# Optimization experiments

Hardware: AMD Instinct MI355X
Metric: run time of the kernel (lower is better)

The kernel has to match this reference:

```python
import jax, jax.numpy as jnp
import numpy as np

T, HID, H, HKV, D = 4096, 2048, 16, 2, 128
EPS = 1e-6


def setup_inputs() -> dict:
    key = jax.random.key(0)
    ks = jax.random.split(key, 5)
    hidden_states = jax.random.normal(ks[0], (T, HID), dtype=jnp.float32)
    # rope angles: build realistic cos/sin from positions and inv-freqs
    inv_freq = 1.0 / (10000.0 ** (jnp.arange(0, D, 2, dtype=jnp.float32) / D))
    ang = jnp.arange(T, dtype=jnp.float32)[:, None] * inv_freq[None, :]  # [T, D/2]
    ang = jnp.concatenate([ang, ang], axis=-1)  # [T, D]
    cos, sin = jnp.cos(ang), jnp.sin(ang)
    w_qkv = jax.random.normal(ks[1], (HID, (2 * H + 2 * HKV) * D), dtype=jnp.float32) * (HID ** -0.5)
    w_o = jax.random.normal(ks[2], (H * D, HID), dtype=jnp.float32) * ((H * D) ** -0.5)
    q_norm_w = jnp.ones((D,), dtype=jnp.float32)
    k_norm_w = jnp.ones((D,), dtype=jnp.float32)
    return {"hidden_states": hidden_states, "cos": cos, "sin": sin,
            "w_qkv": w_qkv, "w_o": w_o, "q_norm_w": q_norm_w, "k_norm_w": k_norm_w}


def _rms_norm(x, w):
    var = jnp.mean(x * x, axis=-1, keepdims=True)
    return x * jax.lax.rsqrt(var + EPS) * w


def _rotate_half(x):
    x1, x2 = x[..., : D // 2], x[..., D // 2:]
    return jnp.concatenate([-x2, x1], axis=-1)


def _rope(x, cos, sin):
    # x: [T, h, D]; cos/sin: [T, D]
    return x * cos[:, None, :] + _rotate_half(x) * sin[:, None, :]


def reference(hidden_states, cos, sin, w_qkv, w_o, q_norm_w, k_norm_w):
    qkv = hidden_states @ w_qkv  # [T, (2H+2HKV)*D]
    q_sz, kv_sz = 2 * H * D, HKV * D
    # packed query+gate: view as [T, H, 2D], first half query, second half gate
    qg = qkv[:, :q_sz].reshape(T, H, 2 * D)
    q, gate = qg[..., :D], qg[..., D:]
    k = qkv[:, q_sz:q_sz + kv_sz].reshape(T, HKV, D)
    v = qkv[:, q_sz + kv_sz:].reshape(T, HKV, D)
    q = _rms_norm(q, q_norm_w)
    k = _rms_norm(k, k_norm_w)
    q = _rope(q, cos, sin)
    k = _rope(k, cos, sin)
    # GQA: expand kv heads to H
    rep = H // HKV
    k = jnp.repeat(k, rep, axis=1)  # [T, H, D]
    v = jnp.repeat(v, rep, axis=1)
    scale = D ** -0.5
    scores = jnp.einsum('thd,shd->hts', q, k) * scale  # [H, T, T]
    causal = jnp.tril(jnp.ones((T, T), dtype=bool))
    scores = jnp.where(causal[None], scores, jnp.finfo(scores.dtype).min)
    probs = jax.nn.softmax(scores, axis=-1)
    attn = jnp.einsum('hts,shd->thd', probs, v)  # [T, H, D]
    out = attn.reshape(T, H * D) * jax.nn.sigmoid(gate.reshape(T, H * D))
    return out @ w_o
```

## Files before the change

kernel.cpp:

```cpp
#include <hip/hip_runtime.h>
#include <hip/hip_bf16.h>
#include <math.h>


namespace {
constexpr int kT   = 4096;
constexpr int kHid = 2048;
constexpr int kH   = 16;
constexpr int kHkv = 2;
constexpr int kD   = 128;
constexpr int kNqkv = (2 * kH + 2 * kHkv) * kD;
constexpr int kQsz  = 2 * kH * kD;
constexpr int kRowU = kNqkv * 2;
constexpr float kEps = 1e-6f;
constexpr float kScale = 0.08838834764831845f;
}

typedef __attribute__((ext_vector_type(8))) short short8;
typedef __attribute__((ext_vector_type(4))) float floatx4;

__device__ inline unsigned short f2bf(float x) {
  unsigned u = __float_as_uint(x);
  u = (u + 0x7fffu + ((u >> 16) & 1u)) >> 16;
  return (unsigned short)u;
}

__device__ inline void gload_lds16(const void* g, void* l) {
  typedef const __attribute__((address_space(1))) unsigned GQ;
  typedef __attribute__((address_space(3))) unsigned LQ;
  __builtin_amdgcn_global_load_lds((GQ*)g, (LQ*)l, 16, 0, 0);
}

__global__ __launch_bounds__(256)
void cvt_bf16(const float* __restrict__ in, unsigned short* __restrict__ out,
              long nelem) {
  long i = ((long)blockIdx.x * 256 + threadIdx.x) * 4;
  if (i >= nelem) return;
  float4 v = *(const float4*)(in + i);
  unsigned long long p = (unsigned long long)f2bf(v.x) |
                         ((unsigned long long)f2bf(v.y) << 16) |
                         ((unsigned long long)f2bf(v.z) << 32) |
                         ((unsigned long long)f2bf(v.w) << 48);
  *(unsigned long long*)(out + i) = p;
}

__global__ __launch_bounds__(256)
void transpose_cvt(const float* __restrict__ in, unsigned short* __restrict__ out,
                   int R, int C) {
  __shared__ float t[32][33];
  const int bx = blockIdx.x * 32;
  const int by = blockIdx.y * 32;
  const int x = threadIdx.x & 31, y = threadIdx.x >> 5;
#pragma unroll
  for (int j = 0; j < 4; ++j)
    t[y * 4 + j][x] = in[(long)(by + y * 4 + j) * C + bx + x];
  __syncthreads();
#pragma unroll
  for (int j = 0; j < 4; ++j)
    out[(long)(bx + y * 4 + j) * R + by + x] = f2bf(t[x][y * 4 + j]);
}

__global__ __launch_bounds__(256)
void vt_transpose(const float* __restrict__ qkv, unsigned short* __restrict__ VtG) {
  __shared__ float t[32][33];
  const int t0 = blockIdx.x * 32;
  const int c0 = blockIdx.y * 32;
  const int x = threadIdx.x & 31, y = threadIdx.x >> 5;
#pragma unroll
  for (int j = 0; j < 4; ++j)
    t[y * 4 + j][x] = qkv[(long)(t0 + y * 4 + j) * kNqkv + 4352 + c0 + x];
  __syncthreads();
#pragma unroll
  for (int j = 0; j < 4; ++j)
    VtG[(long)(c0 + y * 4 + j) * kT + t0 + x] = f2bf(t[x][y * 4 + j]);
}

__global__ __launch_bounds__(256)
void gemm_bf16(const unsigned short* __restrict__ A,
               const unsigned short* __restrict__ Bt, float* __restrict__ C,
               int M, int N, int K) {
  __shared__ __align__(16) unsigned short As[128 * 32];
  __shared__ __align__(16) unsigned short Bs[128 * 32];
  const int tid = threadIdx.x;
  const int lane = tid & 63;
  const int w = tid >> 6;
  const int wr = w >> 1, wc = w & 1;
  const int n = lane & 15;
  const int quad = lane >> 4;
  const long bm = (long)blockIdx.x * 128, bn = (long)blockIdx.y * 128;

  floatx4 acc[4][4];
  floatx4 zero = {0.f, 0.f, 0.f, 0.f};
#pragma unroll
  for (int a = 0; a < 4; ++a)
#pragma unroll
    for (int b = 0; b < 4; ++b) acc[a][b] = zero;

  for (int k0 = 0; k0 < K; k0 += 32) {
    __syncthreads();
#pragma unroll
    for (int it = 0; it < 2; ++it) {
      int ci = (w * 2 + it) * 64 + lane;
      int r = ci >> 2, c = ci & 3;
      int cg = c ^ ((r >> 1) & 3);
      gload_lds16(A + (bm + r) * (long)K + k0 + cg * 8, As + (w * 2 + it) * 512);
      gload_lds16(Bt + (bn + r) * (long)K + k0 + cg * 8, Bs + (w * 2 + it) * 512);
    }
    __syncthreads();

    short8 af[4], bf[4];
#pragma unroll
    for (int a = 0; a < 4; ++a) {
      int m = wr * 64 + a * 16 + n;
      af[a] = *(const short8*)(As + m * 32 + (quad ^ ((m >> 1) & 3)) * 8);
    }
#pragma unroll
    for (int b = 0; b < 4; ++b) {
      int nn = wc * 64 + b * 16 + n;
      bf[b] = *(const short8*)(Bs + nn * 32 + (quad ^ ((nn >> 1) & 3)) * 8);
    }
#pragma unroll
    for (int a = 0; a < 4; ++a)
#pragma unroll
      for (int b = 0; b < 4; ++b)
        acc[a][b] = __builtin_amdgcn_mfma_f32_16x16x32_bf16(af[a], bf[b], acc[a][b], 0, 0, 0);
  }
#pragma unroll
  for (int a = 0; a < 4; ++a)
#pragma unroll
    for (int b = 0; b < 4; ++b)
#pragma unroll
      for (int r = 0; r < 4; ++r)
        C[(bm + wr * 64 + a * 16 + quad * 4 + r) * (long)N + bn + wc * 64 + b * 16 + n] =
            acc[a][b][r];
}

__global__ __launch_bounds__(128)
void norm_rope_cvt(float* qkv, const float* __restrict__ cosb,
                   const float* __restrict__ sinb, const float* __restrict__ qw,
                   const float* __restrict__ kw) {
  unsigned short* qkvu = (unsigned short*)qkv;
  const int blk = blockIdx.x;
  const int t = blk / 18;
  const int h = blk % 18;
  const int i = threadIdx.x;

  const bool isq = (h < kH);
  const long base = (long)t * kNqkv + (isq ? h * 2 * kD : kQsz + (h - kH) * kD);
  float x = qkv[base + i];
  float v = x * x;
#pragma unroll
  for (int off = 1; off < 64; off <<= 1) v += __shfl_xor(v, off, 64);
  __shared__ float wsum[2];
  if ((i & 63) == 0) wsum[i >> 6] = v;
  __syncthreads();
  float rms = rsqrtf((wsum[0] + wsum[1]) * (1.0f / kD) + kEps);
  float nv = x * rms * (isq ? qw[i] : kw[i]);
  __shared__ float nb[128];
  nb[i] = nv;
  __syncthreads();
  float rot = (i < 64) ? -nb[i + 64] : nb[i - 64];
  float ro = nv * cosb[t * kD + i] + rot * sinb[t * kD + i];
  if (isq) {
    float g = qkv[base + kD + i];
    qkv[base + kD + i] = 1.0f / (1.0f + __expf(-g));
    qkvu[(long)t * kRowU + 512 * h + i] = f2bf(ro);
  } else {
    qkvu[(long)t * kRowU + 8192 + 256 * (h - kH) + i] = f2bf(ro);
  }
}

__global__ __launch_bounds__(256, 4)
void flash_attn_mfma(const unsigned short* qkvu, const float* qkvf,
                     const unsigned short* VtG, unsigned short* __restrict__ og) {
  __shared__ __align__(16) unsigned short Ks[64 * 128];
  __shared__ __align__(16) unsigned short Vt[128 * 64];

  const int tid = threadIdx.x;
  const int lane = tid & 63;
  const int w = tid >> 6;
  const int n = lane & 15;
  const int quad = lane >> 4;
  const int g = blockIdx.x;
  const int m = g & 63;
  const int bm = (m & 1) ? 63 - (m >> 1) : (m >> 1);
  const int h = g >> 6;
  const int hk = h >> 3;
  const int q0 = bm * 64;

  short8 qf[4];
  {
    const unsigned short* qrow = qkvu + (long)(q0 + 16 * w + n) * kRowU + 512 * h;
#pragma unroll
    for (int ks = 0; ks < 4; ++ks)
      qf[ks] = *(const short8*)(qrow + 32 * ks + 8 * quad);
  }
  short8 lfrag;
  {
    short o = (n == 0) ? (short)0x3F80 : (short)0;
    lfrag = (short8){o, o, o, o, o, o, o, o};
  }

  floatx4 O[8];
  floatx4 zero = {0.f, 0.f, 0.f, 0.f};
#pragma unroll
  for (int dt = 0; dt < 8; ++dt) O[dt] = zero;
  floatx4 Ol = zero;

  for (int kn = 0; kn <= bm; ++kn) {
    __syncthreads();
#pragma unroll
    for (int it = 0; it < 4; ++it) {
      int pc = (w * 4 + it) * 64 + lane;
      int r = pc >> 4, c = pc & 15;
      int lc = c ^ (r & 15);
      gload_lds16(qkvu + (long)(kn * 64 + r) * kRowU + 8192 + 256 * hk + 8 * lc,
                  Ks + (w * 4 + it) * 512);
    }
#pragma unroll
    for (int it = 0; it < 4; ++it) {
      int pc = (w * 4 + it) * 64 + lane;
      int d = pc >> 3, c = pc & 7;
      int lc = c ^ (d & 7);
      gload_lds16(VtG + (long)hk * (128 * kT) + (long)d * kT + kn * 64 + 8 * lc,
                  Vt + (w * 4 + it) * 512);
    }
    __syncthreads();

    floatx4 S[4];
#pragma unroll
    for (int ct = 0; ct < 4; ++ct) S[ct] = zero;
#pragma unroll
    for (int ks = 0; ks < 4; ++ks) {
#pragma unroll
      for (int ct = 0; ct < 4; ++ct) {
        int row = 16 * ct + n;
        short8 kf = *(const short8*)(Ks + row * 128 + ((4 * ks + quad) ^ n) * 8);
        S[ct] = __builtin_amdgcn_mfma_f32_16x16x32_bf16(qf[ks], kf, S[ct], 0, 0, 0);
      }
    }
    __syncthreads();

    unsigned short* Ps = Ks;
    const bool diag = (kn == bm);
    const int hi = n >> 3, lo = n & 7;
#pragma unroll
    for (int r = 0; r < 4; ++r) {
      int iloc = 16 * w + quad * 4 + r;
      float p0 = __expf(S[0][r] * kScale);
      float p1 = __expf(S[1][r] * kScale);
      float p2 = __expf(S[2][r] * kScale);
      float p3 = __expf(S[3][r] * kScale);
      if (diag) {
        if (n > iloc) p0 = 0.f;
        if (16 + n > iloc) p1 = 0.f;
        if (32 + n > iloc) p2 = 0.f;
        if (48 + n > iloc) p3 = 0.f;
      }
      int prow = 16 * w + quad * 4 + r;
      int sw = prow & 7;
      Ps[prow * 128 + (((0 + hi) ^ sw) << 3) + lo] = f2bf(p0);
      Ps[prow * 128 + (((2 + hi) ^ sw) << 3) + lo] = f2bf(p1);
      Ps[prow * 128 + (((4 + hi) ^ sw) << 3) + lo] = f2bf(p2);
      Ps[prow * 128 + (((6 + hi) ^ sw) << 3) + lo] = f2bf(p3);
    }
    __asm__ volatile("s_waitcnt lgkmcnt(0)" ::: "memory");

#pragma unroll
    for (int ks = 0; ks < 2; ++ks) {
      int rr = 16 * w + n;
      short8 pf = *(const short8*)(Ps + rr * 128 + (((4 * ks + quad) ^ (rr & 7)) << 3));
      Ol = __builtin_amdgcn_mfma_f32_16x16x32_bf16(pf, lfrag, Ol, 0, 0, 0);
#pragma unroll
      for (int dt = 0; dt < 8; ++dt) {
        int d = 16 * dt + n;
        short8 vf = *(const short8*)(Vt + d * 64 + (((4 * ks + quad) ^ (d & 7)) << 3));
        O[dt] = __builtin_amdgcn_mfma_f32_16x16x32_bf16(pf, vf, O[dt], 0, 0, 0);
      }
    }
  }

#pragma unroll
  for (int r = 0; r < 4; ++r) {
    float l = __shfl(Ol[r], quad << 4, 64);
    float inv = 1.0f / l;
    int row = q0 + 16 * w + quad * 4 + r;
#pragma unroll
    for (int dt = 0; dt < 8; ++dt) {
      int col = 16 * dt + n;
      float gte = qkvf[(long)row * kNqkv + 256 * h + 128 + col];
      og[(long)row * kHid + 128 * h + col] = f2bf(O[dt][r] * inv * gte);
    }
  }
}

extern "C" void kernel_launch(void* const* d_in, const int* in_sizes, int n_in,
                              void* d_out, int out_size, void* d_ws, size_t ws_size,
                              hipStream_t stream) {
  (void)in_sizes; (void)n_in; (void)out_size; (void)ws_size;
  const float* hs   = (const float*)d_in[0];
  const float* cosb = (const float*)d_in[1];
  const float* sinb = (const float*)d_in[2];
  const float* wqkv = (const float*)d_in[3];
  const float* wo   = (const float*)d_in[4];
  const float* qw   = (const float*)d_in[5];
  const float* kw   = (const float*)d_in[6];
  float* out = (float*)d_out;

  char* ws = (char*)d_ws;
  float* qkv = (float*)ws;
  unsigned short* hsb = (unsigned short*)(ws + 75497472);
  unsigned short* og  = hsb;
  unsigned short* wt  = (unsigned short*)(ws + 92274688);
  unsigned short* VtG = wt;

  cvt_bf16<<<dim3(8192), 256, 0, stream>>>(hs, hsb, (long)kT * kHid);
  transpose_cvt<<<dim3(kNqkv / 32, kHid / 32), 256, 0, stream>>>(wqkv, wt, kHid, kNqkv);
  gemm_bf16<<<dim3(kT / 128, kNqkv / 128), 256, 0, stream>>>(hsb, wt, qkv, kT, kNqkv, kHid);
  vt_transpose<<<dim3(kT / 32, 8), 256, 0, stream>>>(qkv, VtG);
  norm_rope_cvt<<<dim3(kT * 18), 128, 0, stream>>>(qkv, cosb, sinb, qw, kw);
  flash_attn_mfma<<<dim3(kT / 64 * kH), 256, 0, stream>>>((const unsigned short*)qkv, qkv, VtG, og);
  transpose_cvt<<<dim3(kHid / 32, kHid / 32), 256, 0, stream>>>(wo, wt, kHid, kHid);
  gemm_bf16<<<dim3(kT / 128, kHid / 128), 256, 0, stream>>>(og, wt, out, kT, kHid, kHid);
}
```

Baseline: 551.7 us.

## Double GEMM K-tile and widen attention query tile to 128 rows

The GEMM now stages 64-wide K slices per iteration with an 8-way XOR swizzle, which halves the number of barrier pairs per output tile. The attention kernel handles 128 query rows per block, two 16-row MFMA tiles per wave, so each K/V tile loaded into LDS feeds twice as many queries. Block order is changed to head-fastest with the longest causal rows scheduled first. The cost is more registers per thread (the occupancy hint of 4 is removed) and half as many attention blocks, which can hurt load balance and latency hiding.

```diff
diff --git a/kernel.cpp b/kernel.cpp
--- a/kernel.cpp
+++ b/kernel.cpp
@@ -79,8 +79,8 @@
 void gemm_bf16(const unsigned short* __restrict__ A,
                const unsigned short* __restrict__ Bt, float* __restrict__ C,
                int M, int N, int K) {
-  __shared__ __align__(16) unsigned short As[128 * 32];
-  __shared__ __align__(16) unsigned short Bs[128 * 32];
+  __shared__ __align__(16) unsigned short As[128 * 64];
+  __shared__ __align__(16) unsigned short Bs[128 * 64];
   const int tid = threadIdx.x;
   const int lane = tid & 63;
   const int w = tid >> 6;
@@ -96,34 +96,37 @@
 #pragma unroll
     for (int b = 0; b < 4; ++b) acc[a][b] = zero;
 
-  for (int k0 = 0; k0 < K; k0 += 32) {
-    __syncthreads();
-#pragma unroll
-    for (int it = 0; it < 2; ++it) {
-      int ci = (w * 2 + it) * 64 + lane;
-      int r = ci >> 2, c = ci & 3;
-      int cg = c ^ ((r >> 1) & 3);
-      gload_lds16(A + (bm + r) * (long)K + k0 + cg * 8, As + (w * 2 + it) * 512);
-      gload_lds16(Bt + (bn + r) * (long)K + k0 + cg * 8, Bs + (w * 2 + it) * 512);
-    }
-    __syncthreads();
-
-    short8 af[4], bf[4];
-#pragma unroll
-    for (int a = 0; a < 4; ++a) {
-      int m = wr * 64 + a * 16 + n;
-      af[a] = *(const short8*)(As + m * 32 + (quad ^ ((m >> 1) & 3)) * 8);
-    }
-#pragma unroll
-    for (int b = 0; b < 4; ++b) {
-      int nn = wc * 64 + b * 16 + n;
-      bf[b] = *(const short8*)(Bs + nn * 32 + (quad ^ ((nn >> 1) & 3)) * 8);
-    }
-#pragma unroll
-    for (int a = 0; a < 4; ++a)
-#pragma unroll
-      for (int b = 0; b < 4; ++b)
-        acc[a][b] = __builtin_amdgcn_mfma_f32_16x16x32_bf16(af[a], bf[b], acc[a][b], 0, 0, 0);
+  for (int k0 = 0; k0 < K; k0 += 64) {
+    __syncthreads();
+#pragma unroll
+    for (int it = 0; it < 4; ++it) {
+      int ci = it * 256 + tid;
+      int r = ci >> 3, c = ci & 7;
+      int cg = c ^ (r & 7);
+      gload_lds16(A + (bm + r) * (long)K + k0 + cg * 8, As + (it * 256 + w * 64) * 8);
+      gload_lds16(Bt + (bn + r) * (long)K + k0 + cg * 8, Bs + (it * 256 + w * 64) * 8);
+    }
+    __syncthreads();
+
+#pragma unroll
+    for (int ks = 0; ks < 2; ++ks) {
+      short8 af[4], bf[4];
+#pragma unroll
+      for (int a = 0; a < 4; ++a) {
+        int m = wr * 64 + a * 16 + n;
+        af[a] = *(const short8*)(As + m * 64 + ((4 * ks + quad) ^ (m & 7)) * 8);
+      }
+#pragma unroll
+      for (int b = 0; b < 4; ++b) {
+        int nn = wc * 64 + b * 16 + n;
+        bf[b] = *(const short8*)(Bs + nn * 64 + ((4 * ks + quad) ^ (nn & 7)) * 8);
+      }
+#pragma unroll
+      for (int a = 0; a < 4; ++a)
+#pragma unroll
+        for (int b = 0; b < 4; ++b)
+          acc[a][b] = __builtin_amdgcn_mfma_f32_16x16x32_bf16(af[a], bf[b], acc[a][b], 0, 0, 0);
+    }
   }
 #pragma unroll
   for (int a = 0; a < 4; ++a)
@@ -170,7 +173,7 @@
   }
 }
 
-__global__ __launch_bounds__(256, 4)
+__global__ __launch_bounds__(256)
 void flash_attn_mfma(const unsigned short* qkvu, const float* qkvf,
                      const unsigned short* VtG, unsigned short* __restrict__ og) {
   __shared__ __align__(16) unsigned short Ks[64 * 128];
@@ -182,18 +185,19 @@
   const int n = lane & 15;
   const int quad = lane >> 4;
   const int g = blockIdx.x;
-  const int m = g & 63;
-  const int bm = (m & 1) ? 63 - (m >> 1) : (m >> 1);
-  const int h = g >> 6;
+  const int h = g & 15;
+  const int bm = 31 - (g >> 4);
   const int hk = h >> 3;
-  const int q0 = bm * 64;
-
-  short8 qf[4];
-  {
-    const unsigned short* qrow = qkvu + (long)(q0 + 16 * w + n) * kRowU + 512 * h;
+  const int q0 = bm * 128;
+
+  short8 qf[2][4];
+#pragma unroll
+  for (int mt = 0; mt < 2; ++mt) {
+    const unsigned short* qrow =
+        qkvu + (long)(q0 + 32 * w + 16 * mt + n) * kRowU + 512 * h;
 #pragma unroll
     for (int ks = 0; ks < 4; ++ks)
-      qf[ks] = *(const short8*)(qrow + 32 * ks + 8 * quad);
+      qf[mt][ks] = *(const short8*)(qrow + 32 * ks + 8 * quad);
   }
   short8 lfrag;
   {
@@ -201,13 +205,18 @@
     lfrag = (short8){o, o, o, o, o, o, o, o};
   }
 
-  floatx4 O[8];
+  floatx4 O[2][8];
+  floatx4 Ol[2];
   floatx4 zero = {0.f, 0.f, 0.f, 0.f};
 #pragma unroll
-  for (int dt = 0; dt < 8; ++dt) O[dt] = zero;
-  floatx4 Ol = zero;
-
-  for (int kn = 0; kn <= bm; ++kn) {
+  for (int mt = 0; mt < 2; ++mt) {
+    Ol[mt] = zero;
+#pragma unroll
+    for (int dt = 0; dt < 8; ++dt) O[mt][dt] = zero;
+  }
+
+  const int kn_end = 2 * bm + 1;
+  for (int kn = 0; kn <= kn_end; ++kn) {
     __syncthreads();
 #pragma unroll
     for (int it = 0; it < 4; ++it) {
@@ -227,69 +236,81 @@
     }
     __syncthreads();
 
-    floatx4 S[4];
-#pragma unroll
-    for (int ct = 0; ct < 4; ++ct) S[ct] = zero;
+    floatx4 S[2][4];
+#pragma unroll
+    for (int mt = 0; mt < 2; ++mt)
+#pragma unroll
+      for (int ct = 0; ct < 4; ++ct) S[mt][ct] = zero;
 #pragma unroll
     for (int ks = 0; ks < 4; ++ks) {
 #pragma unroll
       for (int ct = 0; ct < 4; ++ct) {
         int row = 16 * ct + n;
         short8 kf = *(const short8*)(Ks + row * 128 + ((4 * ks + quad) ^ n) * 8);
-        S[ct] = __builtin_amdgcn_mfma_f32_16x16x32_bf16(qf[ks], kf, S[ct], 0, 0, 0);
+        S[0][ct] = __builtin_amdgcn_mfma_f32_16x16x32_bf16(qf[0][ks], kf, S[0][ct], 0, 0, 0);
+        S[1][ct] = __builtin_amdgcn_mfma_f32_16x16x32_bf16(qf[1][ks], kf, S[1][ct], 0, 0, 0);
       }
     }
     __syncthreads();
 
     unsigned short* Ps = Ks;
-    const bool diag = (kn == bm);
+    const bool needmask = (kn >= 2 * bm);
+    const int jbase = (kn - 2 * bm) * 64;
     const int hi = n >> 3, lo = n & 7;
 #pragma unroll
-    for (int r = 0; r < 4; ++r) {
-      int iloc = 16 * w + quad * 4 + r;
-      float p0 = __expf(S[0][r] * kScale);
-      float p1 = __expf(S[1][r] * kScale);
-      float p2 = __expf(S[2][r] * kScale);
-      float p3 = __expf(S[3][r] * kScale);
-      if (diag) {
-        if (n > iloc) p0 = 0.f;
-        if (16 + n > iloc) p1 = 0.f;
-        if (32 + n > iloc) p2 = 0.f;
-        if (48 + n > iloc) p3 = 0.f;
-      }
-      int prow = 16 * w + quad * 4 + r;
-      int sw = prow & 7;
-      Ps[prow * 128 + (((0 + hi) ^ sw) << 3) + lo] = f2bf(p0);
-      Ps[prow * 128 + (((2 + hi) ^ sw) << 3) + lo] = f2bf(p1);
-      Ps[prow * 128 + (((4 + hi) ^ sw) << 3) + lo] = f2bf(p2);
-      Ps[prow * 128 + (((6 + hi) ^ sw) << 3) + lo] = f2bf(p3);
+    for (int mt = 0; mt < 2; ++mt) {
+#pragma unroll
+      for (int r = 0; r < 4; ++r) {
+        int prow = 32 * w + 16 * mt + quad * 4 + r;
+        float p0 = __expf(S[mt][0][r] * kScale);
+        float p1 = __expf(S[mt][1][r] * kScale);
+        float p2 = __expf(S[mt][2][r] * kScale);
+        float p3 = __expf(S[mt][3][r] * kScale);
+        if (needmask) {
+          if (jbase + n > prow) p0 = 0.f;
+          if (jbase + 16 + n > prow) p1 = 0.f;
+          if (jbase + 32 + n > prow) p2 = 0.f;
+          if (jbase + 48 + n > prow) p3 = 0.f;
+        }
+        int sw = prow & 7;
+        Ps[prow * 64 + (((0 + hi) ^ sw) << 3) + lo] = f2bf(p0);
+        Ps[prow * 64 + (((2 + hi) ^ sw) << 3) + lo] = f2bf(p1);
+        Ps[prow * 64 + (((4 + hi) ^ sw) << 3) + lo] = f2bf(p2);
+        Ps[prow * 64 + (((6 + hi) ^ sw) << 3) + lo] = f2bf(p3);
+      }
     }
     __asm__ volatile("s_waitcnt lgkmcnt(0)" ::: "memory");
 
 #pragma unroll
     for (int ks = 0; ks < 2; ++ks) {
-      int rr = 16 * w + n;
-      short8 pf = *(const short8*)(Ps + rr * 128 + (((4 * ks + quad) ^ (rr & 7)) << 3));
-      Ol = __builtin_amdgcn_mfma_f32_16x16x32_bf16(pf, lfrag, Ol, 0, 0, 0);
+      int r0 = 32 * w + n, r1 = 32 * w + 16 + n;
+      short8 pf0 = *(const short8*)(Ps + r0 * 64 + (((4 * ks + quad) ^ (r0 & 7)) << 3));
+      short8 pf1 = *(const short8*)(Ps + r1 * 64 + (((4 * ks + quad) ^ (r1 & 7)) << 3));
+      Ol[0] = __builtin_amdgcn_mfma_f32_16x16x32_bf16(pf0, lfrag, Ol[0], 0, 0, 0);
+      Ol[1] = __builtin_amdgcn_mfma_f32_16x16x32_bf16(pf1, lfrag, Ol[1], 0, 0, 0);
 #pragma unroll
       for (int dt = 0; dt < 8; ++dt) {
         int d = 16 * dt + n;
         short8 vf = *(const short8*)(Vt + d * 64 + (((4 * ks + quad) ^ (d & 7)) << 3));
-        O[dt] = __builtin_amdgcn_mfma_f32_16x16x32_bf16(pf, vf, O[dt], 0, 0, 0);
-      }
-    }
-  }
-
-#pragma unroll
-  for (int r = 0; r < 4; ++r) {
-    float l = __shfl(Ol[r], quad << 4, 64);
-    float inv = 1.0f / l;
-    int row = q0 + 16 * w + quad * 4 + r;
-#pragma unroll
-    for (int dt = 0; dt < 8; ++dt) {
-      int col = 16 * dt + n;
-      float gte = qkvf[(long)row * kNqkv + 256 * h + 128 + col];
-      og[(long)row * kHid + 128 * h + col] = f2bf(O[dt][r] * inv * gte);
+        O[0][dt] = __builtin_amdgcn_mfma_f32_16x16x32_bf16(pf0, vf, O[0][dt], 0, 0, 0);
+        O[1][dt] = __builtin_amdgcn_mfma_f32_16x16x32_bf16(pf1, vf, O[1][dt], 0, 0, 0);
+      }
+    }
+  }
+
+#pragma unroll
+  for (int mt = 0; mt < 2; ++mt) {
+#pragma unroll
+    for (int r = 0; r < 4; ++r) {
+      float l = __shfl(Ol[mt][r], quad << 4, 64);
+      float inv = 1.0f / l;
+      int row = q0 + 32 * w + 16 * mt + quad * 4 + r;
+#pragma unroll
+      for (int dt = 0; dt < 8; ++dt) {
+        int col = 16 * dt + n;
+        float gte = qkvf[(long)row * kNqkv + 256 * h + 128 + col];
+        og[(long)row * kHid + 128 * h + col] = f2bf(O[mt][dt][r] * inv * gte);
+      }
     }
   }
 }
@@ -319,7 +340,7 @@
   gemm_bf16<<<dim3(kT / 128, kNqkv / 128), 256, 0, stream>>>(hsb, wt, qkv, kT, kNqkv, kHid);
   vt_transpose<<<dim3(kT / 32, 8), 256, 0, stream>>>(qkv, VtG);
   norm_rope_cvt<<<dim3(kT * 18), 128, 0, stream>>>(qkv, cosb, sinb, qw, kw);
-  flash_attn_mfma<<<dim3(kT / 64 * kH), 256, 0, stream>>>((const unsigned short*)qkv, qkv, VtG, og);
+  flash_attn_mfma<<<dim3(kT / 128 * kH), 256, 0, stream>>>((const unsigned short*)qkv, qkv, VtG, og);
   transpose_cvt<<<dim3(kHid / 32, kHid / 32), 256, 0, stream>>>(wo, wt, kHid, kHid);
   gemm_bf16<<<dim3(kT / 128, kHid / 128), 256, 0, stream>>>(og, wt, out, kT, kHid, kHid);
 }
```

New measurement: 504.6 us. 1.09x faster.
